# Optimization experiments

Hardware: AMD Instinct MI355X
Metric: run time of the kernel (lower is better)

## Reference

```python
import jax, jax.numpy as jnp
import numpy as np
import math

N, E = 50000, 800000
NFEAT, HID, NCLASS = 512, 96, 64
NUM_LAYERS = 8
ALPHA, THETA = 0.1, 0.5


def setup_inputs() -> dict:
    key = jax.random.key(0)
    ks = jax.random.split(key, 8)
    x = jax.random.normal(ks[0], (N, NFEAT), dtype=jnp.float32)
    # dense_to_sparse(adj_t) -> edge_index; weights are discarded by the module,
    # so propagation uses unit edge weights. We generate the edge list directly.
    edge_index = jax.random.randint(ks[1], (2, E), 0, N, dtype=jnp.int32)
    s_in = 1.0 / math.sqrt(NFEAT)
    s_hid = 1.0 / math.sqrt(HID)
    W_in = jax.random.uniform(ks[2], (NFEAT, HID), jnp.float32, -s_in, s_in)
    b_in = jax.random.uniform(ks[3], (HID,), jnp.float32, -s_in, s_in)
    conv_W = jax.random.uniform(ks[4], (NUM_LAYERS, HID, HID), jnp.float32, -s_hid, s_hid)
    W_out = jax.random.uniform(ks[5], (HID, NCLASS), jnp.float32, -s_hid, s_hid)
    b_out = jax.random.uniform(ks[6], (NCLASS,), jnp.float32, -s_hid, s_hid)
    return {"x": x, "edge_index": edge_index, "W_in": W_in, "b_in": b_in,
            "conv_W": conv_W, "W_out": W_out, "b_out": b_out}


def reference(x, edge_index, W_in, b_in, conv_W, W_out, b_out):
    # Eval mode: dropout is identity.
    src, dst = edge_index[0], edge_index[1]
    h = jax.nn.relu(x @ W_in + b_in)          # [N, HID]
    x0 = h
    for layer in range(NUM_LAYERS):
        beta = math.log(THETA / (layer + 1) + 1.0)
        # sparse propagation: out[i] = sum over edges (j -> i) of h[j]
        agg = jax.ops.segment_sum(h[src], dst, num_segments=N)   # [N, HID]
        hc = (1.0 - ALPHA) * agg + ALPHA * x0                    # initial residual
        h = jax.nn.relu((1.0 - beta) * hc + beta * (hc @ conv_W[layer]))
    out = h @ W_out + b_out                   # [N, NCLASS]
    return jax.nn.log_softmax(out, axis=-1)
```

## Files before the change

### kernel.cpp

```cpp
#include <hip/hip_runtime.h>
#include <math.h>

#define N_NODES 50000
#define N_EDGES 800000
#define NFEAT   512
#define HID     96
#define NCLASS  64
#define NUM_LAYERS 8
#define ALPHA   0.1f
#define NSB     49
#define NBB     196

typedef __attribute__((ext_vector_type(8))) short short8;
typedef __attribute__((ext_vector_type(4))) float f32x4;

__device__ __forceinline__ unsigned short f2bf(float f) {
    unsigned int u = __float_as_uint(f);
    unsigned int r = u + 0x7FFF + ((u >> 16) & 1);
    return (unsigned short)(r >> 16);
}
__device__ __forceinline__ float bflo(unsigned int u) { return __uint_as_float(u << 16); }
__device__ __forceinline__ float bfhi(unsigned int u) { return __uint_as_float(u & 0xFFFF0000u); }
__device__ __forceinline__ float bf2f(short s) {
    return __uint_as_float(((unsigned int)(unsigned short)s) << 16);
}

__device__ __forceinline__ void gload16(const float* g, float* l) {
    __builtin_amdgcn_global_load_lds(
        (const __attribute__((address_space(1))) void*)g,
        (__attribute__((address_space(3))) void*)l, 16, 0, 0);
}

__global__ void hist_kernel(const int* __restrict__ dst, int* __restrict__ deg) {
    int e = blockIdx.x * blockDim.x + threadIdx.x;
    if (e < N_EDGES) atomicAdd(&deg[dst[e]], 1);
}

__global__ void scan1_kernel(const int* __restrict__ deg, int* __restrict__ row_start,
                             int* __restrict__ blk_sum) {
    __shared__ int sd[1024];
    int t = threadIdx.x;
    int i = blockIdx.x * 1024 + t;
    int v = (i < N_NODES) ? ((deg[i] + 3) & ~3) : 0;
    sd[t] = v;
    __syncthreads();
    for (int off = 1; off < 1024; off <<= 1) {
        int tv = (t >= off) ? sd[t - off] : 0;
        __syncthreads();
        sd[t] += tv;
        __syncthreads();
    }
    if (i < N_NODES) row_start[i] = sd[t] - v;
    if (t == 1023) blk_sum[blockIdx.x] = sd[1023];
}

__global__ void scan2_kernel(const int* __restrict__ blk_sum, int* __restrict__ blk_off) {
    if (threadIdx.x == 0) {
        int acc = 0;
        for (int b = 0; b < NSB; b++) { blk_off[b] = acc; acc += blk_sum[b]; }
    }
}

__global__ void scan3_kernel(int* __restrict__ row_start, const int* __restrict__ blk_off) {
    int i = blockIdx.x * 1024 + threadIdx.x;
    if (i < N_NODES) row_start[i] += blk_off[blockIdx.x];
}

__global__ void fill_kernel(const int* __restrict__ src, const int* __restrict__ dst,
                            const int* __restrict__ row_start, int* __restrict__ cursor,
                            int* __restrict__ csr_src) {
    int e = blockIdx.x * blockDim.x + threadIdx.x;
    if (e < N_EDGES) {
        int d = dst[e];
        int pos = row_start[d] + atomicAdd(&cursor[d], 1);
        csr_src[pos] = src[e];
    }
}

__global__ void pad_kernel(const int* __restrict__ deg, const int* __restrict__ row_start,
                           int* __restrict__ csr_src) {
    int n = blockIdx.x * blockDim.x + threadIdx.x;
    if (n < N_NODES) {
        int d = deg[n], pd = (d + 3) & ~3, rs = row_start[n];
        for (int p = d; p < pd; p++) csr_src[rs + p] = N_NODES;
    }
}

__global__ __launch_bounds__(256) void bin_hist2_kernel(
        const int* __restrict__ deg, int* __restrict__ node_rank,
        int* __restrict__ blk_bin_cnt) {
    __shared__ int lh[64];
    int t = threadIdx.x;
    if (t < 64) lh[t] = 0;
    __syncthreads();
    int n = blockIdx.x * 256 + t;
    if (n < N_NODES) {
        int nq = (deg[n] + 3) >> 2; if (nq > 63) nq = 63;
        node_rank[n] = atomicAdd(&lh[nq], 1);
    }
    __syncthreads();
    if (t < 64) blk_bin_cnt[blockIdx.x * 64 + t] = lh[t];
}

__global__ void bin_offsets_kernel(const int* __restrict__ blk_bin_cnt,
                                   int* __restrict__ blk_bin_off,
                                   int* __restrict__ bin_base) {
    __shared__ int tot[64];
    int b = threadIdx.x;
    int acc = 0;
    for (int blk = 0; blk < NBB; blk++) {
        blk_bin_off[blk * 64 + b] = acc;
        acc += blk_bin_cnt[blk * 64 + b];
    }
    tot[b] = acc;
    __syncthreads();
    if (b == 0) {
        int a = 0;
        for (int i = 63; i >= 0; i--) { bin_base[i] = a; a += tot[i]; }
    }
}

__global__ __launch_bounds__(256) void bin_place_kernel(
        const int* __restrict__ deg, const int* __restrict__ node_rank,
        const int* __restrict__ blk_bin_off, const int* __restrict__ bin_base,
        int* __restrict__ perm) {
    int n = blockIdx.x * 256 + threadIdx.x;
    if (n < N_NODES) {
        int nq = (deg[n] + 3) >> 2; if (nq > 63) nq = 63;
        perm[bin_base[nq] + blk_bin_off[blockIdx.x * 64 + nq] + node_rank[n]] = n;
    }
}

__global__ void zero_dummy_kernel(short* __restrict__ h0, short* __restrict__ hb,
                                  short* __restrict__ hc) {
    int t = threadIdx.x;
    if (t < HID) {
        h0[(size_t)N_NODES * HID + t] = 0;
        hb[(size_t)N_NODES * HID + t] = 0;
        hc[(size_t)N_NODES * HID + t] = 0;
    }
}

__global__ void convert_win_kernel(const float* __restrict__ W, short* __restrict__ Wt) {
    int t = blockIdx.x * 256 + threadIdx.x;
    int lane = t & 63;
    int n    = (t >> 6) % 6;
    int ks   = t / 384;
    int quad = lane >> 4, l16 = lane & 15;
    short8 v;
#pragma unroll
    for (int j = 0; j < 8; j++)
        v[j] = (short)f2bf(W[(size_t)(ks * 32 + quad * 8 + j) * HID + n * 16 + l16]);
    *(short8*)&Wt[(size_t)t * 8] = v;
}

__global__ void convert_wout_kernel(const float* __restrict__ W, short* __restrict__ Wt) {
    int n = blockIdx.x;
    int k = threadIdx.x;
    Wt[(size_t)n * HID + k] = (short)f2bf(W[(size_t)k * NCLASS + n]);
}

__global__ void convert_wconv_kernel(const float* __restrict__ W, short* __restrict__ Wc) {
    int n = blockIdx.x;
    int l = blockIdx.y;
    int k = threadIdx.x;
    Wc[(size_t)l * HID * HID + (size_t)n * HID + k] =
        (short)f2bf(W[(size_t)l * HID * HID + (size_t)k * HID + n]);
}

__global__ __launch_bounds__(256) void gemm_in_kernel(
        const float* __restrict__ x, const short* __restrict__ WtT,
        const float* __restrict__ b, short* __restrict__ h0) {
    __shared__ __align__(16) float As[2][4096];
    int tid  = threadIdx.x;
    int wave = tid >> 6, lane = tid & 63;
    int quad = lane >> 4, l16 = lane & 15;
    int row0 = blockIdx.x * 64;

    const float* gsrc[4];
#pragma unroll
    for (int r = 0; r < 4; r++) {
        int rl  = r * 4 + (lane >> 4);
        int row = row0 + wave * 16 + rl;
        if (row >= N_NODES) row = N_NODES - 1;
        int c2s = (lane & 15) ^ rl;
        gsrc[r] = &x[(size_t)row * NFEAT + c2s * 4];
    }

    f32x4 acc[6];
#pragma unroll
    for (int n = 0; n < 6; n++) acc[n] = (f32x4){0.f, 0.f, 0.f, 0.f};

    {
        float* lb = &As[0][wave * 1024];
#pragma unroll
        for (int r = 0; r < 4; r++) gload16(gsrc[r], lb + r * 256);
    }

#pragma unroll
    for (int c = 0; c < 8; c++) {
        __syncthreads();
        if (c < 7) {
            float* nb = &As[(c + 1) & 1][wave * 1024];
#pragma unroll
            for (int r = 0; r < 4; r++) gload16(gsrc[r] + (c + 1) * 64, nb + r * 256);
        }
        const float* cb = &As[c & 1][wave * 1024 + l16 * 64];
#pragma unroll
        for (int s = 0; s < 2; s++) {
            int c2a = s * 8 + quad * 2;
            f32x4 fa = *(const f32x4*)&cb[((c2a    ) ^ l16) * 4];
            f32x4 fb = *(const f32x4*)&cb[((c2a + 1) ^ l16) * 4];
            union { short8 sv; uint4 u; } af;
            af.u.x = (unsigned)f2bf(fa[0]) | ((unsigned)f2bf(fa[1]) << 16);
            af.u.y = (unsigned)f2bf(fa[2]) | ((unsigned)f2bf(fa[3]) << 16);
            af.u.z = (unsigned)f2bf(fb[0]) | ((unsigned)f2bf(fb[1]) << 16);
            af.u.w = (unsigned)f2bf(fb[2]) | ((unsigned)f2bf(fb[3]) << 16);
            int ks = c * 2 + s;
            const short* bbase = &WtT[(size_t)(ks * 6) * 512 + lane * 8];
#pragma unroll
            for (int n = 0; n < 6; n++) {
                short8 bfrag = *(const short8*)&bbase[n * 512];
                acc[n] = __builtin_amdgcn_mfma_f32_16x16x32_bf16(af.sv, bfrag, acc[n], 0, 0, 0);
            }
        }
    }

    int row0w = row0 + wave * 16;
#pragma unroll
    for (int n = 0; n < 6; n++) {
        int col = n * 16 + l16;
        float bias = b[col];
#pragma unroll
        for (int r = 0; r < 4; r++) {
            int grow = row0w + quad * 4 + r;
            if (grow < N_NODES) {
                float v = acc[n][r] + bias;
                v = v > 0.f ? v : 0.f;
                h0[(size_t)grow * HID + col] = (short)f2bf(v);
            }
        }
    }
}

__global__ __launch_bounds__(384) void layer_kernel(
        const short* __restrict__ h_in, const short* __restrict__ x0bf,
        const int* __restrict__ row_start, const int* __restrict__ deg,
        const int* __restrict__ csr_src, const int* __restrict__ perm,
        const short* __restrict__ Wc, float beta, short* __restrict__ h_out) {
    __shared__ short As[32][104];
    __shared__ int   snode[32];
    int tid = threadIdx.x;
    int tx = tid % 12;
    int ty = tid / 12;
    int idx = blockIdx.x * 32 + ty;
    bool valid = idx < N_NODES;
    int node = valid ? perm[idx] : (N_NODES - 1);
    if (tx == 0) snode[ty] = valid ? node : -1;

    int s = row_start[node];
    int d = deg[node];
    int nq = (d + 3) >> 2;
    const int4* c4 = (const int4*)(csr_src + s);
    float acc[8];
#pragma unroll
    for (int j = 0; j < 8; j++) acc[j] = 0.f;
    for (int i = 0; i < nq; i++) {
        int4 idxv = c4[i];
        uint4 a0 = *(const uint4*)&h_in[(size_t)idxv.x * HID + tx * 8];
        uint4 a1 = *(const uint4*)&h_in[(size_t)idxv.y * HID + tx * 8];
        uint4 a2 = *(const uint4*)&h_in[(size_t)idxv.z * HID + tx * 8];
        uint4 a3 = *(const uint4*)&h_in[(size_t)idxv.w * HID + tx * 8];
        acc[0] += bflo(a0.x) + bflo(a1.x) + bflo(a2.x) + bflo(a3.x);
        acc[1] += bfhi(a0.x) + bfhi(a1.x) + bfhi(a2.x) + bfhi(a3.x);
        acc[2] += bflo(a0.y) + bflo(a1.y) + bflo(a2.y) + bflo(a3.y);
        acc[3] += bfhi(a0.y) + bfhi(a1.y) + bfhi(a2.y) + bfhi(a3.y);
        acc[4] += bflo(a0.z) + bflo(a1.z) + bflo(a2.z) + bflo(a3.z);
        acc[5] += bfhi(a0.z) + bfhi(a1.z) + bfhi(a2.z) + bfhi(a3.z);
        acc[6] += bflo(a0.w) + bflo(a1.w) + bflo(a2.w) + bflo(a3.w);
        acc[7] += bfhi(a0.w) + bfhi(a1.w) + bfhi(a2.w) + bfhi(a3.w);
    }
    uint4 xq = *(const uint4*)&x0bf[(size_t)node * HID + tx * 8];
    float hc[8];
    hc[0] = (1.f - ALPHA) * acc[0] + ALPHA * bflo(xq.x);
    hc[1] = (1.f - ALPHA) * acc[1] + ALPHA * bfhi(xq.x);
    hc[2] = (1.f - ALPHA) * acc[2] + ALPHA * bflo(xq.y);
    hc[3] = (1.f - ALPHA) * acc[3] + ALPHA * bfhi(xq.y);
    hc[4] = (1.f - ALPHA) * acc[4] + ALPHA * bflo(xq.z);
    hc[5] = (1.f - ALPHA) * acc[5] + ALPHA * bfhi(xq.z);
    hc[6] = (1.f - ALPHA) * acc[6] + ALPHA * bflo(xq.w);
    hc[7] = (1.f - ALPHA) * acc[7] + ALPHA * bfhi(xq.w);
    {
        uint4 pk;
        pk.x = (unsigned)f2bf(hc[0]) | ((unsigned)f2bf(hc[1]) << 16);
        pk.y = (unsigned)f2bf(hc[2]) | ((unsigned)f2bf(hc[3]) << 16);
        pk.z = (unsigned)f2bf(hc[4]) | ((unsigned)f2bf(hc[5]) << 16);
        pk.w = (unsigned)f2bf(hc[6]) | ((unsigned)f2bf(hc[7]) << 16);
        *(uint4*)&As[ty][tx * 8] = pk;
    }
    __syncthreads();

    int wave = tid >> 6, lane = tid & 63;
    int quad = lane >> 4, l16 = lane & 15;
    int rt = wave & 1;
    int ct0 = (wave >> 1) * 2, ct1 = ct0 + 1;

    f32x4 g0 = (f32x4){0.f,0.f,0.f,0.f}, g1 = (f32x4){0.f,0.f,0.f,0.f};
#pragma unroll
    for (int ks = 0; ks < 3; ks++) {
        short8 afrag = *(const short8*)&As[rt * 16 + l16][ks * 32 + quad * 8];
        short8 b0 = *(const short8*)&Wc[(size_t)(ct0 * 16 + l16) * HID + ks * 32 + quad * 8];
        short8 b1 = *(const short8*)&Wc[(size_t)(ct1 * 16 + l16) * HID + ks * 32 + quad * 8];
        g0 = __builtin_amdgcn_mfma_f32_16x16x32_bf16(afrag, b0, g0, 0, 0, 0);
        g1 = __builtin_amdgcn_mfma_f32_16x16x32_bf16(afrag, b1, g1, 0, 0, 0);
    }
    float ob = 1.0f - beta;
#pragma unroll
    for (int r = 0; r < 4; r++) {
        int lrow = rt * 16 + quad * 4 + r;
        int nd = snode[lrow];
        if (nd >= 0) {
            int c0 = ct0 * 16 + l16;
            int c1 = ct1 * 16 + l16;
            float v0 = ob * bf2f(As[lrow][c0]) + beta * g0[r];
            float v1 = ob * bf2f(As[lrow][c1]) + beta * g1[r];
            v0 = v0 > 0.f ? v0 : 0.f;
            v1 = v1 > 0.f ? v1 : 0.f;
            h_out[(size_t)nd * HID + c0] = (short)f2bf(v0);
            h_out[(size_t)nd * HID + c1] = (short)f2bf(v1);
        }
    }
}

__global__ __launch_bounds__(256) void out_kernel(
        const short* __restrict__ h_bf, const short* __restrict__ Wt,
        const float* __restrict__ b, float* __restrict__ out) {
    int tid = threadIdx.x;
    int wave = tid >> 6, lane = tid & 63;
    int quad = lane >> 4, l16 = lane & 15;
    int row0 = blockIdx.x * 64 + wave * 16;

    f32x4 acc[4];
#pragma unroll
    for (int n = 0; n < 4; n++) acc[n] = (f32x4){0.f, 0.f, 0.f, 0.f};

    int arow = row0 + l16; if (arow > N_NODES) arow = N_NODES;
#pragma unroll
    for (int ks = 0; ks < 3; ks++) {
        short8 afrag = *(const short8*)&h_bf[(size_t)arow * HID + ks * 32 + quad * 8];
#pragma unroll
        for (int n = 0; n < 4; n++) {
            short8 bfrag = *(const short8*)&Wt[(size_t)(n * 16 + l16) * HID + ks * 32 + quad * 8];
            acc[n] = __builtin_amdgcn_mfma_f32_16x16x32_bf16(afrag, bfrag, acc[n], 0, 0, 0);
        }
    }
#pragma unroll
    for (int n = 0; n < 4; n++) {
        float bias = b[n * 16 + l16];
#pragma unroll
        for (int r = 0; r < 4; r++) acc[n][r] += bias;
    }
#pragma unroll
    for (int r = 0; r < 4; r++) {
        float m = acc[0][r];
        m = fmaxf(m, acc[1][r]); m = fmaxf(m, acc[2][r]); m = fmaxf(m, acc[3][r]);
#pragma unroll
        for (int off = 1; off < 16; off <<= 1) m = fmaxf(m, __shfl_xor(m, off));
        float s = __expf(acc[0][r] - m) + __expf(acc[1][r] - m)
                + __expf(acc[2][r] - m) + __expf(acc[3][r] - m);
#pragma unroll
        for (int off = 1; off < 16; off <<= 1) s += __shfl_xor(s, off);
        float lse = m + __logf(s);
        int grow = row0 + quad * 4 + r;
        if (grow < N_NODES) {
#pragma unroll
            for (int n = 0; n < 4; n++)
                out[(size_t)grow * NCLASS + n * 16 + l16] = acc[n][r] - lse;
        }
    }
}

extern "C" void kernel_launch(void* const* d_in, const int* in_sizes, int n_in,
                              void* d_out, int out_size, void* d_ws, size_t ws_size,
                              hipStream_t stream) {
    const float* x      = (const float*)d_in[0];
    const int*   ei     = (const int*)d_in[1];
    const int*   srcp   = ei;
    const int*   dstp   = ei + N_EDGES;
    const float* W_in   = (const float*)d_in[2];
    const float* b_in   = (const float*)d_in[3];
    const float* conv_W = (const float*)d_in[4];
    const float* W_out  = (const float*)d_in[5];
    const float* b_out  = (const float*)d_in[6];
    float* out = (float*)d_out;

    short* h0  = (short*)d_ws;
    short* h_b = h0  + (size_t)(N_NODES + 1) * HID;
    short* h_c = h_b + (size_t)(N_NODES + 1) * HID;
    short* Wt_in  = h_c + (size_t)(N_NODES + 1) * HID;
    short* Wt_out = Wt_in + (size_t)HID * NFEAT;
    short* Wc     = Wt_out + (size_t)NCLASS * HID;
    int* deg        = (int*)(Wc + (size_t)NUM_LAYERS * HID * HID);
    int* row_start  = deg + N_NODES;
    int* cursor     = row_start + N_NODES;
    int* blk_sum    = cursor + N_NODES;
    int* blk_off    = blk_sum + 64;
    int* bin_base   = blk_off + 64;
    int* node_rank  = bin_base + 64;
    int* perm       = node_rank + N_NODES;
    int* blk_bin_cnt= perm + N_NODES;
    int* blk_bin_off= blk_bin_cnt + NBB * 64;
    int* csr_src    = blk_bin_off + NBB * 64;

    hipMemsetAsync(deg,    0, N_NODES * sizeof(int), stream);
    hipMemsetAsync(cursor, 0, N_NODES * sizeof(int), stream);
    hist_kernel<<<(N_EDGES + 255) / 256, 256, 0, stream>>>(dstp, deg);
    scan1_kernel<<<NSB, 1024, 0, stream>>>(deg, row_start, blk_sum);
    scan2_kernel<<<1, 64, 0, stream>>>(blk_sum, blk_off);
    scan3_kernel<<<NSB, 1024, 0, stream>>>(row_start, blk_off);
    fill_kernel<<<(N_EDGES + 255) / 256, 256, 0, stream>>>(srcp, dstp, row_start, cursor, csr_src);
    pad_kernel<<<(N_NODES + 255) / 256, 256, 0, stream>>>(deg, row_start, csr_src);
    bin_hist2_kernel<<<NBB, 256, 0, stream>>>(deg, node_rank, blk_bin_cnt);
    bin_offsets_kernel<<<1, 64, 0, stream>>>(blk_bin_cnt, blk_bin_off, bin_base);
    bin_place_kernel<<<NBB, 256, 0, stream>>>(deg, node_rank, blk_bin_off, bin_base, perm);

    convert_win_kernel<<<24, 256, 0, stream>>>(W_in, Wt_in);
    convert_wout_kernel<<<NCLASS, HID, 0, stream>>>(W_out, Wt_out);
    convert_wconv_kernel<<<dim3(HID, NUM_LAYERS), HID, 0, stream>>>(conv_W, Wc);
    gemm_in_kernel<<<(N_NODES + 63) / 64, 256, 0, stream>>>(x, Wt_in, b_in, h0);
    zero_dummy_kernel<<<1, 128, 0, stream>>>(h0, h_b, h_c);

    short* cur = h0;
    short* nxt = h_b;
    for (int l = 0; l < NUM_LAYERS; l++) {
        float beta = logf(0.5f / (float)(l + 1) + 1.0f);
        layer_kernel<<<(N_NODES + 31) / 32, 384, 0, stream>>>(
            cur, h0, row_start, deg, csr_src, perm, Wc + (size_t)l * HID * HID, beta, nxt);
        cur = nxt;
        nxt = (cur == h_b) ? h_c : h_b;
    }

    out_kernel<<<(N_NODES + 63) / 64, 256, 0, stream>>>(cur, Wt_out, b_out, out);
}
```

Baseline: 538.1 us.

## Fuse scan offset kernels, use per-wave vmcnt waits, and packed bf16 conversion

Removes the single-thread scan2 kernel by having each scan3 block compute its own prefix offset with a wave shuffle reduction, which saves one launch. In the input GEMM, the per-chunk __syncthreads is replaced with explicit s_waitcnt vmcnt waits, because each wave loads only its own LDS region. Float-to-bf16 packing switches to the library's paired round-to-nearest conversion, which can map to a hardware packed-convert instruction. Dropping the block barrier leans on the assumption that each wave reads only its own LDS slice.

Result: no change. 538.9 us (+0.2%).

```diff
diff --git a/kernel.cpp b/kernel.cpp
--- a/kernel.cpp
+++ b/kernel.cpp
@@ -1,4 +1,5 @@
 #include <hip/hip_runtime.h>
+#include <hip/hip_bf16.h>
 #include <math.h>
 
 #define N_NODES 50000
@@ -19,6 +20,10 @@
     unsigned int r = u + 0x7FFF + ((u >> 16) & 1);
     return (unsigned short)(r >> 16);
 }
+__device__ __forceinline__ unsigned cvtpk(float a, float b) {
+    __hip_bfloat162 h = __float22bfloat162_rn(float2{a, b});
+    return *reinterpret_cast<unsigned*>(&h);
+}
 __device__ __forceinline__ float bflo(unsigned int u) { return __uint_as_float(u << 16); }
 __device__ __forceinline__ float bfhi(unsigned int u) { return __uint_as_float(u & 0xFFFF0000u); }
 __device__ __forceinline__ float bf2f(short s) {
@@ -54,16 +59,18 @@
     if (t == 1023) blk_sum[blockIdx.x] = sd[1023];
 }
 
-__global__ void scan2_kernel(const int* __restrict__ blk_sum, int* __restrict__ blk_off) {
-    if (threadIdx.x == 0) {
-        int acc = 0;
-        for (int b = 0; b < NSB; b++) { blk_off[b] = acc; acc += blk_sum[b]; }
-    }
-}
-
-__global__ void scan3_kernel(int* __restrict__ row_start, const int* __restrict__ blk_off) {
-    int i = blockIdx.x * 1024 + threadIdx.x;
-    if (i < N_NODES) row_start[i] += blk_off[blockIdx.x];
+__global__ void scan3_kernel(int* __restrict__ row_start, const int* __restrict__ blk_sum) {
+    __shared__ int soff;
+    int t = threadIdx.x;
+    if (t < 64) {
+        int v = (t < blockIdx.x) ? blk_sum[t] : 0;
+#pragma unroll
+        for (int off = 1; off < 64; off <<= 1) v += __shfl_xor(v, off);
+        if (t == 0) soff = v;
+    }
+    __syncthreads();
+    int i = blockIdx.x * 1024 + t;
+    if (i < N_NODES) row_start[i] += soff;
 }
 
 __global__ void fill_kernel(const int* __restrict__ src, const int* __restrict__ dst,
@@ -191,31 +198,33 @@
 #pragma unroll
     for (int n = 0; n < 6; n++) acc[n] = (f32x4){0.f, 0.f, 0.f, 0.f};
 
-    {
-        float* lb = &As[0][wave * 1024];
-#pragma unroll
-        for (int r = 0; r < 4; r++) gload16(gsrc[r], lb + r * 256);
-    }
+    float* lb0 = &As[0][wave * 1024];
+    float* lb1 = &As[1][wave * 1024];
+#pragma unroll
+    for (int r = 0; r < 4; r++) gload16(gsrc[r], lb0 + r * 256);
 
 #pragma unroll
     for (int c = 0; c < 8; c++) {
-        __syncthreads();
         if (c < 7) {
-            float* nb = &As[(c + 1) & 1][wave * 1024];
+            float* nb = ((c + 1) & 1) ? lb1 : lb0;
 #pragma unroll
             for (int r = 0; r < 4; r++) gload16(gsrc[r] + (c + 1) * 64, nb + r * 256);
-        }
-        const float* cb = &As[c & 1][wave * 1024 + l16 * 64];
+            asm volatile("s_waitcnt vmcnt(4)" ::: "memory");
+        } else {
+            asm volatile("s_waitcnt vmcnt(0)" ::: "memory");
+        }
+        __builtin_amdgcn_sched_barrier(0);
+        const float* cb = ((c & 1) ? lb1 : lb0) + l16 * 64;
 #pragma unroll
         for (int s = 0; s < 2; s++) {
             int c2a = s * 8 + quad * 2;
             f32x4 fa = *(const f32x4*)&cb[((c2a    ) ^ l16) * 4];
             f32x4 fb = *(const f32x4*)&cb[((c2a + 1) ^ l16) * 4];
             union { short8 sv; uint4 u; } af;
-            af.u.x = (unsigned)f2bf(fa[0]) | ((unsigned)f2bf(fa[1]) << 16);
-            af.u.y = (unsigned)f2bf(fa[2]) | ((unsigned)f2bf(fa[3]) << 16);
-            af.u.z = (unsigned)f2bf(fb[0]) | ((unsigned)f2bf(fb[1]) << 16);
-            af.u.w = (unsigned)f2bf(fb[2]) | ((unsigned)f2bf(fb[3]) << 16);
+            af.u.x = cvtpk(fa[0], fa[1]);
+            af.u.y = cvtpk(fa[2], fa[3]);
+            af.u.z = cvtpk(fb[0], fb[1]);
+            af.u.w = cvtpk(fb[2], fb[3]);
             int ks = c * 2 + s;
             const short* bbase = &WtT[(size_t)(ks * 6) * 512 + lane * 8];
 #pragma unroll
@@ -292,10 +301,10 @@
     hc[7] = (1.f - ALPHA) * acc[7] + ALPHA * bfhi(xq.w);
     {
         uint4 pk;
-        pk.x = (unsigned)f2bf(hc[0]) | ((unsigned)f2bf(hc[1]) << 16);
-        pk.y = (unsigned)f2bf(hc[2]) | ((unsigned)f2bf(hc[3]) << 16);
-        pk.z = (unsigned)f2bf(hc[4]) | ((unsigned)f2bf(hc[5]) << 16);
-        pk.w = (unsigned)f2bf(hc[6]) | ((unsigned)f2bf(hc[7]) << 16);
+        pk.x = cvtpk(hc[0], hc[1]);
+        pk.y = cvtpk(hc[2], hc[3]);
+        pk.z = cvtpk(hc[4], hc[5]);
+        pk.w = cvtpk(hc[6], hc[7]);
         *(uint4*)&As[ty][tx * 8] = pk;
     }
     __syncthreads();
@@ -404,8 +413,7 @@
     int* row_start  = deg + N_NODES;
     int* cursor     = row_start + N_NODES;
     int* blk_sum    = cursor + N_NODES;
-    int* blk_off    = blk_sum + 64;
-    int* bin_base   = blk_off + 64;
+    int* bin_base   = blk_sum + 64;
     int* node_rank  = bin_base + 64;
     int* perm       = node_rank + N_NODES;
     int* blk_bin_cnt= perm + N_NODES;
@@ -416,8 +424,7 @@
     hipMemsetAsync(cursor, 0, N_NODES * sizeof(int), stream);
     hist_kernel<<<(N_EDGES + 255) / 256, 256, 0, stream>>>(dstp, deg);
     scan1_kernel<<<NSB, 1024, 0, stream>>>(deg, row_start, blk_sum);
-    scan2_kernel<<<1, 64, 0, stream>>>(blk_sum, blk_off);
-    scan3_kernel<<<NSB, 1024, 0, stream>>>(row_start, blk_off);
+    scan3_kernel<<<NSB, 1024, 0, stream>>>(row_start, blk_sum);
     fill_kernel<<<(N_EDGES + 255) / 256, 256, 0, stream>>>(srcp, dstp, row_start, cursor, csr_src);
     pad_kernel<<<(N_NODES + 255) / 256, 256, 0, stream>>>(deg, row_start, csr_src);
     bin_hist2_kernel<<<NBB, 256, 0, stream>>>(deg, node_rank, blk_bin_cnt);
```
